# Optimization experiments

Measured on AMD Instinct MI355X. Metric: run time of the kernel, lower is better.

Reference implementation:

```python
import jax, jax.numpy as jnp
import numpy as np

B, SEQ, NC = 128, 256, 16
IN_SIZE = 256
HID = 256


def setup_inputs() -> dict:
    key = jax.random.key(0)
    ks = jax.random.split(key, 10)
    codes = jax.random.randint(ks[0], (B, SEQ, NC), 0, IN_SIZE + 1)
    mask = jax.random.uniform(ks[1], (B, SEQ, NC), dtype=jnp.float32)
    times = jax.random.uniform(ks[2], (B, SEQ), dtype=jnp.float32)
    s_in = 1.0 / np.sqrt(IN_SIZE)
    s_h = 1.0 / np.sqrt(HID)
    emb = jax.random.normal(ks[3], (IN_SIZE + 1, HID), dtype=jnp.float32)
    emb = emb.at[IN_SIZE].set(0.0)  # padding_idx row
    Wall_w = jax.random.uniform(ks[4], (4 * HID, IN_SIZE), minval=-s_in, maxval=s_in, dtype=jnp.float32)
    Wall_b = jax.random.uniform(ks[5], (4 * HID,), minval=-s_in, maxval=s_in, dtype=jnp.float32)
    Uall_w = jax.random.uniform(ks[6], (4 * HID, HID), minval=-s_h, maxval=s_h, dtype=jnp.float32)
    Uall_b = jax.random.uniform(ks[7], (4 * HID,), minval=-s_h, maxval=s_h, dtype=jnp.float32)
    Wd_w = jax.random.uniform(ks[8], (HID, HID), minval=-s_h, maxval=s_h, dtype=jnp.float32)
    Wd_b = jax.random.uniform(ks[9], (HID,), minval=-s_h, maxval=s_h, dtype=jnp.float32)
    return {"codes": codes, "mask": mask, "times": times, "emb": emb,
            "Wall_w": Wall_w, "Wall_b": Wall_b, "Uall_w": Uall_w, "Uall_b": Uall_b,
            "Wd_w": Wd_w, "Wd_b": Wd_b}


def reference(codes, mask, times, emb, Wall_w, Wall_b, Uall_w, Uall_b, Wd_w, Wd_b):
    # time decay: 1 / log(t + e)
    ts = 1.0 / jnp.log(times + 2.7183)  # [b, seq]
    # visit embedding: masked sum over codes -> [b, seq, hid]
    x = (emb[codes] * mask[..., None]).sum(axis=2)
    # precompute input projection for all steps: [b, seq, 4h]
    xp = jnp.einsum('bsh,gh->bsg', x, Uall_w) + Uall_b
    b = x.shape[0]
    h0 = jnp.zeros((b, HID), dtype=x.dtype)
    c0 = jnp.zeros((b, HID), dtype=x.dtype)

    def step(carry, inp):
        h, c = carry
        xp_s, t_s = inp  # [b,4h], [b]
        c_s1 = jnp.tanh(c @ Wd_w.T + Wd_b)
        c_adj = (c - c_s1) + c_s1 * t_s[:, None]
        outs = h @ Wall_w.T + Wall_b + xp_s
        f, i, o, c_tmp = jnp.split(outs, 4, axis=1)
        f = jax.nn.sigmoid(f)
        i = jax.nn.sigmoid(i)
        o = jax.nn.sigmoid(o)
        c_tmp = jax.nn.sigmoid(c_tmp)
        c_new = f * c_adj + i * c_tmp
        h_new = o * jnp.tanh(c_new)
        return (h_new, c_new), h_new

    _, hs = jax.lax.scan(step, (h0, c0), (xp.transpose(1, 0, 2), ts.T))
    return hs.transpose(1, 0, 2)  # [b, seq, hid]
```

## Files before the change

### kernel.cpp

```cpp
#include <hip/hip_runtime.h>
#include <stdint.h>

#define BATCH 128
#define SEQ   256
#define SEQ1  257
#define NC    16
#define HID   256
#define G4    1024

typedef _Float16 half8 __attribute__((ext_vector_type(8)));
typedef float    f32x4 __attribute__((ext_vector_type(4)));
typedef int      i32x4 __attribute__((ext_vector_type(4)));

#define SWINV 258064.0f
#define SW    (1.f/258064.0f)
#define SWD   (1.f/(2032.f*15.875f))

__device__ __forceinline__ uint16_t f32_to_f16u(float f){
  union { _Float16 h; uint16_t u; } c; c.h = (_Float16)f; return c.u;
}
__device__ __forceinline__ float f16u_to_f32(uint32_t u){
  union { uint16_t u; _Float16 h; } c; c.u = (uint16_t)u; return (float)c.h;
}
__device__ __forceinline__ float rcp_(float x){
#if __has_builtin(__builtin_amdgcn_rcpf)
  return __builtin_amdgcn_rcpf(x);
#else
  float r; asm volatile("v_rcp_f32 %0, %1" : "=v"(r) : "v"(x)); return r;
#endif
}
__device__ __forceinline__ float tanh_(float x){
  x = fminf(fmaxf(x, -15.f), 15.f);
  float e = __expf(2.f * x);
  return (e - 1.f) * rcp_(e + 1.f);
}
__device__ __forceinline__ float sigm_(float x){ return rcp_(1.f + __expf(-x)); }

__device__ __forceinline__ uint32_t q4(const float* s, float sc){
  uint32_t r = 0;
  #pragma unroll
  for (int i = 0; i < 4; i++){
    int q = __float2int_rn(s[i] * sc);
    q = max(-127, min(127, q));
    r |= ((uint32_t)(q & 0xFF)) << (8 * i);
  }
  return r;
}

__global__ __launch_bounds__(256) void prep(
    const int* __restrict__ codes, const float* __restrict__ mask,
    const float* __restrict__ emb,
    const float* __restrict__ Wall_w, const float* __restrict__ Wd_w,
    const float* __restrict__ Uall_w, const float* __restrict__ times,
    uint16_t* __restrict__ xh,
    uint4* __restrict__ wpkB, uint4* __restrict__ wdB,
    uint16_t* __restrict__ uh, float* __restrict__ ts_all,
    int* __restrict__ xpi, int use_xpi)
{
  const int bid = blockIdx.x, t = threadIdx.x;
  if (bid < 1024){
    __shared__ int   scd[32][NC];
    __shared__ float smk[32][NC];
    const int bs0 = bid * 32;
    #pragma unroll
    for (int i = 0; i < 2; i++){
      int idx = t + i * 256;
      int rr = idx >> 4, kk = idx & 15;
      scd[rr][kk] = codes[(size_t)(bs0 + rr) * NC + kk];
      smk[rr][kk] = mask [(size_t)(bs0 + rr) * NC + kk];
    }
    __syncthreads();
    for (int rr = 0; rr < 32; rr++){
      float acc = 0.f;
      #pragma unroll
      for (int k = 0; k < NC; k++)
        acc += emb[(size_t)scd[rr][k] * HID + t] * smk[rr][k];
      xh[(size_t)(bs0 + rr) * HID + t] = f32_to_f16u(acc);
    }
    return;
  }
  int L = (bid - 1024) * 256 + t;
  if (L < 16384){
    int slot = L >> 10, tid = L & 1023;
    int tt = slot >> 2, q = slot & 3;
    int w = tid >> 6, l = tid & 63;
    int c = l & 15, r = l >> 4;
    int row = tt * 256 + w * 16 + c;
    int kb = q * 64 + r * 16;
    const float* src = Wall_w + (size_t)row * 256 + kb;
    uint4 v;
    v.x = q4(src +  0, 2032.f);
    v.y = q4(src +  4, 2032.f);
    v.z = q4(src +  8, 2032.f);
    v.w = q4(src + 12, 2032.f);
    wpkB[L] = v;
  } else if (L < 20480){
    int L2 = L - 16384;
    int q = L2 >> 10, tid = L2 & 1023;
    int w = tid >> 6, l = tid & 63;
    int c = l & 15, r = l >> 4;
    int row = w * 16 + c;
    int kb = q * 64 + r * 16;
    const float* src = Wd_w + (size_t)row * 256 + kb;
    uint4 v;
    v.x = q4(src +  0, 2032.f);
    v.y = q4(src +  4, 2032.f);
    v.z = q4(src +  8, 2032.f);
    v.w = q4(src + 12, 2032.f);
    wdB[L2] = v;
  } else if (L < 282624){
    int i = L - 20480;
    uh[i] = f32_to_f16u(Uall_w[i]);
  } else if (L < 315520){
    int i = L - 282624;
    int b = i / SEQ1, s = i - b * SEQ1;
    ts_all[i] = (s < SEQ) ? (1.f / logf(times[b * SEQ + s] + 2.7183f)) : 0.f;
  } else if (L < 446592 && use_xpi){
    int e = L - 315520;
    int b = e >> 10, k = e & 1023;
    xpi[((size_t)(b * SEQ1 + SEQ)) * G4 + k] = 0;
  }
}

template<bool XPI>
__global__ __launch_bounds__(256, 2) void xp_gemm_mfma(
    const uint16_t* __restrict__ xh, const uint16_t* __restrict__ uh,
    const float* __restrict__ Ub, const float* __restrict__ Wb,
    int* __restrict__ xpi, uint16_t* __restrict__ xpf)
{
  __shared__ _Float16 As[128][40];
  __shared__ _Float16 Bs[128][40];
  const int tid = threadIdx.x;
  const int m0 = blockIdx.y * 128;
  const int u0 = blockIdx.x * 32;
  const int w = tid >> 6, l = tid & 63;
  const int wr = w >> 1, wc = w & 1;
  const int sr0 = tid >> 2, sk0 = (tid & 3) * 8;
  const int brow0 = ((sr0 & 3) << 8) + u0 + (sr0 >> 2);
  const int brow1 = ((sr0 & 3) << 8) + u0 + 16 + (sr0 >> 2);

  f32x4 acc[4][4];
  #pragma unroll
  for (int i = 0; i < 4; i++)
    #pragma unroll
    for (int j = 0; j < 4; j++)
      acc[i][j] = (f32x4){0.f, 0.f, 0.f, 0.f};

  for (int k0 = 0; k0 < 256; k0 += 32){
    uint4 a0 = *(const uint4*)(xh + (size_t)(m0 + sr0) * 256 + k0 + sk0);
    uint4 a1 = *(const uint4*)(xh + (size_t)(m0 + 64 + sr0) * 256 + k0 + sk0);
    uint4 b0 = *(const uint4*)(uh + (size_t)brow0 * 256 + k0 + sk0);
    uint4 b1 = *(const uint4*)(uh + (size_t)brow1 * 256 + k0 + sk0);
    __syncthreads();
    *(uint4*)&As[sr0][sk0]      = a0;
    *(uint4*)&As[64 + sr0][sk0] = a1;
    *(uint4*)&Bs[sr0][sk0]      = b0;
    *(uint4*)&Bs[64 + sr0][sk0] = b1;
    __syncthreads();
    half8 af[4], bf[4];
    #pragma unroll
    for (int i = 0; i < 4; i++)
      af[i] = *(half8*)&As[wr*64 + i*16 + (l & 15)][(l >> 4) * 8];
    #pragma unroll
    for (int j = 0; j < 4; j++)
      bf[j] = *(half8*)&Bs[wc*64 + j*16 + (l & 15)][(l >> 4) * 8];
    #pragma unroll
    for (int i = 0; i < 4; i++)
      #pragma unroll
      for (int j = 0; j < 4; j++)
        acc[i][j] = __builtin_amdgcn_mfma_f32_16x16x32_f16(af[i], bf[j], acc[i][j], 0, 0, 0);
  }

  #pragma unroll
  for (int j = 0; j < 4; j++){
    int ncol = wc*64 + j*16 + (l & 15);
    int g = ncol & 3, u = u0 + (ncol >> 2);
    float bs = Ub[g * 256 + u] + Wb[g * 256 + u];
    int colg = u0 * 4 + ncol;
    #pragma unroll
    for (int i = 0; i < 4; i++){
      #pragma unroll
      for (int r = 0; r < 4; r++){
        int m_e = m0 + wr*64 + i*16 + (l >> 4)*4 + r;
        int bb = m_e >> 8, s = m_e & 255;
        size_t row = (size_t)(bb * SEQ1 + s);
        float v = acc[i][j][r] + bs;
        if (XPI) xpi[row * G4 + colg] = __float2int_rn(v * SWINV);
        else     xpf[row * G4 + colg] = f32_to_f16u(v);
      }
    }
  }
}

template<bool XPI>
__global__ __launch_bounds__(1024, 4) void recurrence(
    const i32x4* __restrict__ wpkB, const i32x4* __restrict__ wdB,
    const float* __restrict__ Wd_b,
    const int* __restrict__ xpi, const uint16_t* __restrict__ xpf,
    const float* __restrict__ ts_all,
    float* __restrict__ out)
{
  const int b = blockIdx.x, tid = threadIdx.x;
  const int l = tid & 63;
  const int c = l & 15, r = l >> 4;
  const int U = (tid >> 6) * 16 + c;

  __shared__ __align__(16) uint32_t h8[2][64];
  __shared__ __align__(16) uint32_t c8[2][64];

  i32x4 ww[4][4];
  #pragma unroll
  for (int t = 0; t < 4; t++)
    #pragma unroll
    for (int q = 0; q < 4; q++)
      ww[t][q] = wpkB[(t * 4 + q) * 1024 + tid];
  i32x4 wd[4];
  #pragma unroll
  for (int q = 0; q < 4; q++) wd[q] = wdB[q * 1024 + tid];

  const float bD  = Wd_b[U];

  if (tid < 128) ((uint32_t*)h8)[tid] = 0u;
  else if (tid < 256) ((uint32_t*)c8)[tid - 128] = 0u;
  __syncthreads();

  const int*      xpi_b = xpi + (size_t)b * SEQ1 * G4;
  const uint16_t* xpf_b = xpf + (size_t)b * SEQ1 * G4;
  const float*    ts_b  = ts_all + (size_t)b * SEQ1;
  float* out_b = out + (size_t)b * SEQ * HID;

  float c_reg = 0.f;
  float hn_prev = 0.f;
  i32x4 xvi;
  uint2 xvf;
  if (XPI) xvi = *(const i32x4*)(xpi_b + (U << 2));
  else     xvf = *(const uint2*)(xpf_b + (U << 2));
  float tsv = ts_b[0];

  for (int s = 0; s < SEQ; s++){
    const int buf = s & 1;

    if (s > 0 && r == 0) out_b[(size_t)(s - 1) * HID + U] = hn_prev;

    i32x4 xni; uint2 xnf;
    if (XPI) xni = *(const i32x4*)(xpi_b + (size_t)(s + 1) * G4 + (U << 2));
    else {
      if (s + 1 < SEQ) xnf = *(const uint2*)(xpf_b + (size_t)(s + 1) * G4 + (U << 2));
      else             xnf = make_uint2(0u, 0u);
    }
    float tsn = ts_b[s + 1];

    const char* hbase = (const char*)&h8[buf][0];
    const char* cbase = (const char*)&c8[buf][0];
    i32x4 hA[4], cA[4];
    #pragma unroll
    for (int q = 0; q < 4; q++){
      hA[q] = *(const i32x4*)(hbase + q * 64 + r * 16);
      cA[q] = *(const i32x4*)(cbase + q * 64 + r * 16);
    }

    i32x4 ad = (i32x4){0, 0, 0, 0};
    #pragma unroll
    for (int q = 0; q < 4; q++)
      ad = __builtin_amdgcn_mfma_i32_16x16x64_i8(cA[q], wd[q], ad, 0, 0, 0);

    i32x4 a0, a1, a2, a3;
    if (XPI){ a0 = xvi; a1 = xvi; a2 = xvi; a3 = xvi; }
    else { a0 = (i32x4){0,0,0,0}; a1 = a0; a2 = a0; a3 = a0; }
    #pragma unroll
    for (int q = 0; q < 4; q++) a0 = __builtin_amdgcn_mfma_i32_16x16x64_i8(hA[q], ww[0][q], a0, 0, 0, 0);
    #pragma unroll
    for (int q = 0; q < 4; q++) a1 = __builtin_amdgcn_mfma_i32_16x16x64_i8(hA[q], ww[1][q], a1, 0, 0, 0);
    #pragma unroll
    for (int q = 0; q < 4; q++) a2 = __builtin_amdgcn_mfma_i32_16x16x64_i8(hA[q], ww[2][q], a2, 0, 0, 0);
    #pragma unroll
    for (int q = 0; q < 4; q++) a3 = __builtin_amdgcn_mfma_i32_16x16x64_i8(hA[q], ww[3][q], a3, 0, 0, 0);

    float pf, pi, po, pc;
    if (XPI){
      pf = (float)a0[0] * SW;
      pi = (float)a1[1] * SW;
      po = (float)a2[2] * SW;
      pc = (float)a3[3] * SW;
    } else {
      pf = (float)a0[0] * SW + f16u_to_f32(xvf.x & 0xffff);
      pi = (float)a1[0] * SW + f16u_to_f32(xvf.x >> 16);
      po = (float)a2[0] * SW + f16u_to_f32(xvf.y & 0xffff);
      pc = (float)a3[0] * SW + f16u_to_f32(xvf.y >> 16);
    }
    float wdot = (float)ad[0] * SWD + bD;

    float fg = sigm_(pf), ig = sigm_(pi), og = sigm_(po), ct = sigm_(pc);
    float cs1  = tanh_(wdot);
    float cadj = (c_reg - cs1) + cs1 * tsv;
    float cn = fg * cadj + ig * ct;
    float hn = og * tanh_(cn);
    c_reg = cn;
    hn_prev = hn;

    if (r == 0){
      int hq = __float2int_rn(hn * 127.f);
      hq = max(-127, min(127, hq));
      float cc = fminf(fmaxf(cn, -7.9f), 7.9f);
      int cq = __float2int_rn(cc * 15.875f);
      ((int8_t*)&h8[buf ^ 1][0])[U] = (int8_t)hq;
      ((int8_t*)&c8[buf ^ 1][0])[U] = (int8_t)cq;
    }
    if (XPI) xvi = xni; else xvf = xnf;
    tsv = tsn;
    __syncthreads();
  }
  if (r == 0) out_b[(size_t)(SEQ - 1) * HID + U] = hn_prev;
}

extern "C" void kernel_launch(void* const* d_in, const int* in_sizes, int n_in,
                              void* d_out, int out_size, void* d_ws, size_t ws_size,
                              hipStream_t stream){
  const int*   codes  = (const int*)  d_in[0];
  const float* mask   = (const float*)d_in[1];
  const float* times  = (const float*)d_in[2];
  const float* emb    = (const float*)d_in[3];
  const float* Wall_w = (const float*)d_in[4];
  const float* Wall_b = (const float*)d_in[5];
  const float* Uall_w = (const float*)d_in[6];
  const float* Uall_b = (const float*)d_in[7];
  const float* Wd_w   = (const float*)d_in[8];
  const float* Wd_b   = (const float*)d_in[9];
  float* out = (float*)d_out;

  char* ws = (char*)d_ws;
  const size_t offWpk = 0;
  const size_t offWd  = 262144;
  const size_t offTs  = 327680;
  const size_t offUh  = 460800;
  const size_t offXh  = 1048576;
  const size_t offXp  = 17825792;
  const size_t xpiBytes = (size_t)BATCH * SEQ1 * G4 * 4;
  const bool use_xpi = (ws_size >= offXp + xpiBytes);

  uint4*    wpkB   = (uint4*)   (ws + offWpk);
  uint4*    wdB    = (uint4*)   (ws + offWd);
  float*    ts_all = (float*)   (ws + offTs);
  uint16_t* uh     = (uint16_t*)(ws + offUh);
  uint16_t* xh     = (uint16_t*)(ws + offXh);
  int*      xpi    = (int*)     (ws + offXp);
  uint16_t* xpf    = (uint16_t*)(ws + offXp);

  hipLaunchKernelGGL(prep, dim3(1024 + 1745), dim3(256), 0, stream,
                     codes, mask, emb, Wall_w, Wd_w, Uall_w, times,
                     xh, wpkB, wdB, uh, ts_all, xpi, (int)use_xpi);
  if (use_xpi){
    hipLaunchKernelGGL((xp_gemm_mfma<true>),  dim3(8, 256), dim3(256), 0, stream,
                       xh, uh, Uall_b, Wall_b, xpi, xpf);
    hipLaunchKernelGGL((recurrence<true>),  dim3(BATCH), dim3(1024), 0, stream,
                       (const i32x4*)wpkB, (const i32x4*)wdB, Wd_b, xpi, xpf, ts_all, out);
  } else {
    hipLaunchKernelGGL((xp_gemm_mfma<false>), dim3(8, 256), dim3(256), 0, stream,
                       xh, uh, Uall_b, Wall_b, xpi, xpf);
    hipLaunchKernelGGL((recurrence<false>), dim3(BATCH), dim3(1024), 0, stream,
                       (const i32x4*)wpkB, (const i32x4*)wdB, Wd_b, xpi, xpf, ts_all, out);
  }
}
```

Measured before the change: 345.9 us.

## Halve recurrence block to 512 threads, each wave computing two 16-unit tiles

The recurrence kernel now runs 8 waves per batch element instead of 16. Each wave owns two 16-unit column tiles, so it keeps twice the int8 weight fragments in registers and issues twice the MFMA work per step. The prep kernel's weight packing is rewritten to match the new tile ownership. The aim is to cut per-step barrier cost and wave scheduling overhead across 256 serial steps. In exchange each wave carries a longer serial chain and higher register pressure.

```diff
diff --git a/kernel.cpp b/kernel.cpp
--- a/kernel.cpp
+++ b/kernel.cpp
@@ -81,11 +81,11 @@
   }
   int L = (bid - 1024) * 256 + t;
   if (L < 16384){
-    int slot = L >> 10, tid = L & 1023;
-    int tt = slot >> 2, q = slot & 3;
+    int slot = L >> 9, tid = L & 511;
+    int tau = slot >> 4, tt = (slot >> 2) & 3, q = slot & 3;
     int w = tid >> 6, l = tid & 63;
     int c = l & 15, r = l >> 4;
-    int row = tt * 256 + w * 16 + c;
+    int row = tt * 256 + w * 32 + tau * 16 + c;
     int kb = q * 64 + r * 16;
     const float* src = Wall_w + (size_t)row * 256 + kb;
     uint4 v;
@@ -96,18 +96,21 @@
     wpkB[L] = v;
   } else if (L < 20480){
     int L2 = L - 16384;
-    int q = L2 >> 10, tid = L2 & 1023;
-    int w = tid >> 6, l = tid & 63;
-    int c = l & 15, r = l >> 4;
-    int row = w * 16 + c;
-    int kb = q * 64 + r * 16;
-    const float* src = Wd_w + (size_t)row * 256 + kb;
-    uint4 v;
-    v.x = q4(src +  0, 2032.f);
-    v.y = q4(src +  4, 2032.f);
-    v.z = q4(src +  8, 2032.f);
-    v.w = q4(src + 12, 2032.f);
-    wdB[L2] = v;
+    if (L2 < 4096){
+      int slot = L2 >> 9, tid = L2 & 511;
+      int tau = slot >> 2, q = slot & 3;
+      int w = tid >> 6, l = tid & 63;
+      int c = l & 15, r = l >> 4;
+      int row = w * 32 + tau * 16 + c;
+      int kb = q * 64 + r * 16;
+      const float* src = Wd_w + (size_t)row * 256 + kb;
+      uint4 v;
+      v.x = q4(src +  0, 2032.f);
+      v.y = q4(src +  4, 2032.f);
+      v.z = q4(src +  8, 2032.f);
+      v.w = q4(src + 12, 2032.f);
+      wdB[L2] = v;
+    }
   } else if (L < 282624){
     int i = L - 20480;
     uh[i] = f32_to_f16u(Uall_w[i]);
@@ -193,8 +196,9 @@
 }
 
 template<bool XPI>
-__global__ __launch_bounds__(1024, 4) void recurrence(
-    const i32x4* __restrict__ wpkB, const i32x4* __restrict__ wdB,
+__global__ __launch_bounds__(512) void recurrence(
+    const i32x4* __restrict__ wpkB,
+    const i32x4* __restrict__ wdB,
     const float* __restrict__ Wd_b,
     const int* __restrict__ xpi, const uint16_t* __restrict__ xpf,
     const float* __restrict__ ts_all,
@@ -203,22 +207,30 @@
   const int b = blockIdx.x, tid = threadIdx.x;
   const int l = tid & 63;
   const int c = l & 15, r = l >> 4;
-  const int U = (tid >> 6) * 16 + c;
+  const int w = tid >> 6;
+  const int U0 = w * 32 + c;
+  const int U1 = U0 + 16;
 
   __shared__ __align__(16) uint32_t h8[2][64];
   __shared__ __align__(16) uint32_t c8[2][64];
 
-  i32x4 ww[4][4];
-  #pragma unroll
-  for (int t = 0; t < 4; t++)
+  i32x4 ww[2][4][4];
+  #pragma unroll
+  for (int tau = 0; tau < 2; tau++)
+    #pragma unroll
+    for (int t = 0; t < 4; t++)
+      #pragma unroll
+      for (int q = 0; q < 4; q++)
+        ww[tau][t][q] = wpkB[(((tau * 4 + t) * 4) + q) * 512 + tid];
+  i32x4 wd[2][4];
+  #pragma unroll
+  for (int tau = 0; tau < 2; tau++)
     #pragma unroll
     for (int q = 0; q < 4; q++)
-      ww[t][q] = wpkB[(t * 4 + q) * 1024 + tid];
-  i32x4 wd[4];
-  #pragma unroll
-  for (int q = 0; q < 4; q++) wd[q] = wdB[q * 1024 + tid];
-
-  const float bD  = Wd_b[U];
+      wd[tau][q] = wdB[(tau * 4 + q) * 512 + tid];
+
+  const float bD0 = Wd_b[U0];
+  const float bD1 = Wd_b[U1];
 
   if (tid < 128) ((uint32_t*)h8)[tid] = 0u;
   else if (tid < 256) ((uint32_t*)c8)[tid - 128] = 0u;
@@ -229,24 +241,36 @@
   const float*    ts_b  = ts_all + (size_t)b * SEQ1;
   float* out_b = out + (size_t)b * SEQ * HID;
 
-  float c_reg = 0.f;
-  float hn_prev = 0.f;
-  i32x4 xvi;
-  uint2 xvf;
-  if (XPI) xvi = *(const i32x4*)(xpi_b + (U << 2));
-  else     xvf = *(const uint2*)(xpf_b + (U << 2));
+  float c_reg0 = 0.f, c_reg1 = 0.f;
+  float hn_prev0 = 0.f, hn_prev1 = 0.f;
+  i32x4 xvi0, xvi1;
+  uint2 xvf0, xvf1;
+  if (XPI){
+    xvi0 = *(const i32x4*)(xpi_b + (U0 << 2));
+    xvi1 = *(const i32x4*)(xpi_b + (U1 << 2));
+  } else {
+    xvf0 = *(const uint2*)(xpf_b + (U0 << 2));
+    xvf1 = *(const uint2*)(xpf_b + (U1 << 2));
+  }
   float tsv = ts_b[0];
 
   for (int s = 0; s < SEQ; s++){
     const int buf = s & 1;
 
-    if (s > 0 && r == 0) out_b[(size_t)(s - 1) * HID + U] = hn_prev;
-
-    i32x4 xni; uint2 xnf;
-    if (XPI) xni = *(const i32x4*)(xpi_b + (size_t)(s + 1) * G4 + (U << 2));
-    else {
-      if (s + 1 < SEQ) xnf = *(const uint2*)(xpf_b + (size_t)(s + 1) * G4 + (U << 2));
-      else             xnf = make_uint2(0u, 0u);
+    if (s > 0 && r == 0){
+      out_b[(size_t)(s - 1) * HID + U0] = hn_prev0;
+      out_b[(size_t)(s - 1) * HID + U1] = hn_prev1;
+    }
+
+    i32x4 xni0, xni1; uint2 xnf0, xnf1;
+    if (XPI){
+      xni0 = *(const i32x4*)(xpi_b + (size_t)(s + 1) * G4 + (U0 << 2));
+      xni1 = *(const i32x4*)(xpi_b + (size_t)(s + 1) * G4 + (U1 << 2));
+    } else {
+      if (s + 1 < SEQ){
+        xnf0 = *(const uint2*)(xpf_b + (size_t)(s + 1) * G4 + (U0 << 2));
+        xnf1 = *(const uint2*)(xpf_b + (size_t)(s + 1) * G4 + (U1 << 2));
+      } else { xnf0 = make_uint2(0u,0u); xnf1 = make_uint2(0u,0u); }
     }
     float tsn = ts_b[s + 1];
 
@@ -259,58 +283,70 @@
       cA[q] = *(const i32x4*)(cbase + q * 64 + r * 16);
     }
 
-    i32x4 ad = (i32x4){0, 0, 0, 0};
-    #pragma unroll
-    for (int q = 0; q < 4; q++)
-      ad = __builtin_amdgcn_mfma_i32_16x16x64_i8(cA[q], wd[q], ad, 0, 0, 0);
-
-    i32x4 a0, a1, a2, a3;
-    if (XPI){ a0 = xvi; a1 = xvi; a2 = xvi; a3 = xvi; }
-    else { a0 = (i32x4){0,0,0,0}; a1 = a0; a2 = a0; a3 = a0; }
-    #pragma unroll
-    for (int q = 0; q < 4; q++) a0 = __builtin_amdgcn_mfma_i32_16x16x64_i8(hA[q], ww[0][q], a0, 0, 0, 0);
-    #pragma unroll
-    for (int q = 0; q < 4; q++) a1 = __builtin_amdgcn_mfma_i32_16x16x64_i8(hA[q], ww[1][q], a1, 0, 0, 0);
-    #pragma unroll
-    for (int q = 0; q < 4; q++) a2 = __builtin_amdgcn_mfma_i32_16x16x64_i8(hA[q], ww[2][q], a2, 0, 0, 0);
-    #pragma unroll
-    for (int q = 0; q < 4; q++) a3 = __builtin_amdgcn_mfma_i32_16x16x64_i8(hA[q], ww[3][q], a3, 0, 0, 0);
-
-    float pf, pi, po, pc;
-    if (XPI){
-      pf = (float)a0[0] * SW;
-      pi = (float)a1[1] * SW;
-      po = (float)a2[2] * SW;
-      pc = (float)a3[3] * SW;
-    } else {
-      pf = (float)a0[0] * SW + f16u_to_f32(xvf.x & 0xffff);
-      pi = (float)a1[0] * SW + f16u_to_f32(xvf.x >> 16);
-      po = (float)a2[0] * SW + f16u_to_f32(xvf.y & 0xffff);
-      pc = (float)a3[0] * SW + f16u_to_f32(xvf.y >> 16);
-    }
-    float wdot = (float)ad[0] * SWD + bD;
-
-    float fg = sigm_(pf), ig = sigm_(pi), og = sigm_(po), ct = sigm_(pc);
-    float cs1  = tanh_(wdot);
-    float cadj = (c_reg - cs1) + cs1 * tsv;
-    float cn = fg * cadj + ig * ct;
-    float hn = og * tanh_(cn);
-    c_reg = cn;
-    hn_prev = hn;
-
-    if (r == 0){
-      int hq = __float2int_rn(hn * 127.f);
-      hq = max(-127, min(127, hq));
-      float cc = fminf(fmaxf(cn, -7.9f), 7.9f);
-      int cq = __float2int_rn(cc * 15.875f);
-      ((int8_t*)&h8[buf ^ 1][0])[U] = (int8_t)hq;
-      ((int8_t*)&c8[buf ^ 1][0])[U] = (int8_t)cq;
-    }
-    if (XPI) xvi = xni; else xvf = xnf;
+    #pragma unroll
+    for (int tau = 0; tau < 2; tau++){
+      i32x4 ad = (i32x4){0, 0, 0, 0};
+      #pragma unroll
+      for (int q = 0; q < 4; q++)
+        ad = __builtin_amdgcn_mfma_i32_16x16x64_i8(cA[q], wd[tau][q], ad, 0, 0, 0);
+
+      i32x4 a0, a1, a2, a3;
+      if (XPI){
+        i32x4 xv = tau ? xvi1 : xvi0;
+        a0 = xv; a1 = xv; a2 = xv; a3 = xv;
+      } else {
+        a0 = (i32x4){0,0,0,0}; a1 = a0; a2 = a0; a3 = a0;
+      }
+      #pragma unroll
+      for (int q = 0; q < 4; q++) a0 = __builtin_amdgcn_mfma_i32_16x16x64_i8(hA[q], ww[tau][0][q], a0, 0, 0, 0);
+      #pragma unroll
+      for (int q = 0; q < 4; q++) a1 = __builtin_amdgcn_mfma_i32_16x16x64_i8(hA[q], ww[tau][1][q], a1, 0, 0, 0);
+      #pragma unroll
+      for (int q = 0; q < 4; q++) a2 = __builtin_amdgcn_mfma_i32_16x16x64_i8(hA[q], ww[tau][2][q], a2, 0, 0, 0);
+      #pragma unroll
+      for (int q = 0; q < 4; q++) a3 = __builtin_amdgcn_mfma_i32_16x16x64_i8(hA[q], ww[tau][3][q], a3, 0, 0, 0);
+
+      float pf, pi, po, pc;
+      if (XPI){
+        pf = (float)a0[0] * SW;
+        pi = (float)a1[1] * SW;
+        po = (float)a2[2] * SW;
+        pc = (float)a3[3] * SW;
+      } else {
+        uint2 xf = tau ? xvf1 : xvf0;
+        pf = (float)a0[0] * SW + f16u_to_f32(xf.x & 0xffff);
+        pi = (float)a1[0] * SW + f16u_to_f32(xf.x >> 16);
+        po = (float)a2[0] * SW + f16u_to_f32(xf.y & 0xffff);
+        pc = (float)a3[0] * SW + f16u_to_f32(xf.y >> 16);
+      }
+      float wdot = (float)ad[0] * SWD + (tau ? bD1 : bD0);
+
+      float fg = sigm_(pf), ig = sigm_(pi), og = sigm_(po), ct = sigm_(pc);
+      float cs1  = tanh_(wdot);
+      float creg = tau ? c_reg1 : c_reg0;
+      float cadj = (creg - cs1) + cs1 * tsv;
+      float cn = fg * cadj + ig * ct;
+      float hn = og * tanh_(cn);
+      if (tau){ c_reg1 = cn; hn_prev1 = hn; } else { c_reg0 = cn; hn_prev0 = hn; }
+
+      if (r == 0){
+        int hq = __float2int_rn(hn * 127.f);
+        hq = max(-127, min(127, hq));
+        float cc = fminf(fmaxf(cn, -7.9f), 7.9f);
+        int cq = __float2int_rn(cc * 15.875f);
+        int U = tau ? U1 : U0;
+        ((int8_t*)&h8[buf ^ 1][0])[U] = (int8_t)hq;
+        ((int8_t*)&c8[buf ^ 1][0])[U] = (int8_t)cq;
+      }
+    }
+    if (XPI){ xvi0 = xni0; xvi1 = xni1; } else { xvf0 = xnf0; xvf1 = xnf1; }
     tsv = tsn;
     __syncthreads();
   }
-  if (r == 0) out_b[(size_t)(SEQ - 1) * HID + U] = hn_prev;
+  if (r == 0){
+    out_b[(size_t)(SEQ - 1) * HID + U0] = hn_prev0;
+    out_b[(size_t)(SEQ - 1) * HID + U1] = hn_prev1;
+  }
 }
 
 extern "C" void kernel_launch(void* const* d_in, const int* in_sizes, int n_in,
@@ -352,12 +388,12 @@
   if (use_xpi){
     hipLaunchKernelGGL((xp_gemm_mfma<true>),  dim3(8, 256), dim3(256), 0, stream,
                        xh, uh, Uall_b, Wall_b, xpi, xpf);
-    hipLaunchKernelGGL((recurrence<true>),  dim3(BATCH), dim3(1024), 0, stream,
+    hipLaunchKernelGGL((recurrence<true>),  dim3(BATCH), dim3(512), 0, stream,
                        (const i32x4*)wpkB, (const i32x4*)wdB, Wd_b, xpi, xpf, ts_all, out);
   } else {
     hipLaunchKernelGGL((xp_gemm_mfma<false>), dim3(8, 256), dim3(256), 0, stream,
                        xh, uh, Uall_b, Wall_b, xpi, xpf);
-    hipLaunchKernelGGL((recurrence<false>), dim3(BATCH), dim3(1024), 0, stream,
+    hipLaunchKernelGGL((recurrence<false>), dim3(BATCH), dim3(512), 0, stream,
                        (const i32x4*)wpkB, (const i32x4*)wdB, Wd_b, xpi, xpf, ts_all, out);
   }
 }
```

New measurement: 359.1 us. 3.8% more time.
